# Kernel optimization log

Hardware: AMD Instinct MI355X
Metric: run time of the kernel (lower is better)

The kernel has to match this reference:

```python
import jax, jax.numpy as jnp
import numpy as np

B, T, C, H, N = 4, 1024, 1024, 16, 64
DW, DA, DV, DG = 64, 64, 64, 160  # LoRA ranks derived from C=1024
LNX_EPS = 0.00064


def layer_norm(h, g, b, eps=1e-5):
    m = h.mean(-1, keepdims=True)
    var = ((h - m) ** 2).mean(-1, keepdims=True)
    return (h - m) * jax.lax.rsqrt(var + eps) * g + b


def token_shift(h):
    # nn.ZeroPad2d((0,0,1,-1)): shift right along T, zero at t=0
    return jnp.pad(h, ((0, 0), (1, 0), (0, 0)))[:, :-1]


def wkv7(r, w, k, v, a, b):
    # RWKV-7 generalized recurrence. Inputs [B,T,C]; w is log-space decay.
    def re(t):
        return t.reshape(B, T, H, N).transpose(1, 0, 2, 3)  # -> [T,B,H,N]
    r, w, k, v, a, b = map(re, (r, w, k, v, a, b))
    dec = jnp.exp(-jnp.exp(w))
    S0 = jnp.zeros((B, H, N, N), r.dtype)  # state: [value_dim, key_dim]
    def step(S, ins):
        r_, d_, k_, v_, a_, b_ = ins
        sa = jnp.einsum('bhij,bhj->bhi', S, a_)
        S = S * d_[:, :, None, :] + sa[..., None] * b_[:, :, None, :] + v_[..., None] * k_[:, :, None, :]
        return S, jnp.einsum('bhij,bhj->bhi', S, r_)
    _, out = jax.lax.scan(step, S0, (r, dec, k, v, a, b))
    return out.transpose(1, 0, 2, 3).reshape(B, T, C)


def _forward(x, v_first, ln1_g, ln1_b, ln2_g, ln2_b, x_r, x_w, x_k_mix, x_v_mix, x_a, x_g,
             w0, w1, w2, a0, a1, a2, v0, v1, v2, g1, g2, k_k, k_a, r_k,
             W_r, W_k, W_v, W_o, lnx_g, lnx_b, xk_c, Wk_ff, Wv_ff):
    # ---- RNW_Tmix (original RWKV-7 path, layer_id > 0) ----
    h = layer_norm(x, ln1_g, ln1_b)
    xx = token_shift(h) - h
    xr = h + xx * x_r
    xw = h + xx * x_w
    xk = h + xx * x_k_mix
    xv = h + xx * x_v_mix
    xa = h + xx * x_a
    xg = h + xx * x_g
    r = xr @ W_r.T
    w = -jax.nn.softplus(-(w0 + jnp.tanh(xw @ w1) @ w2)) - 0.5
    k = xk @ W_k.T
    v = xv @ W_v.T
    v = v + (v_first - v) * jax.nn.sigmoid(v0 + (xv @ v1) @ v2)
    a = jax.nn.sigmoid(a0 + (xa @ a1) @ a2)
    g = jax.nn.sigmoid(xg @ g1) @ g2
    kk = (k * k_k).reshape(B, T, H, N)
    kk = kk / jnp.maximum(jnp.linalg.norm(kk, axis=-1, keepdims=True), 1e-12)
    kk = kk.reshape(B, T, C)
    k = k * (1 + (a - 1) * k_a)
    y = wkv7(r, w, k, v, -kk, kk * a)
    # GroupNorm(H groups of N channels), eps=0.00064
    yg = y.reshape(B, T, H, N)
    m = yg.mean(-1, keepdims=True)
    var = ((yg - m) ** 2).mean(-1, keepdims=True)
    y = ((yg - m) * jax.lax.rsqrt(var + LNX_EPS)).reshape(B, T, C) * lnx_g + lnx_b
    r4 = r.reshape(B, T, H, N)
    k4 = k.reshape(B, T, H, N)
    v4 = v.reshape(B, T, H, N)
    y = y + ((r4 * k4 * r_k).sum(-1, keepdims=True) * v4).reshape(B, T, C)
    x = x + (y * g) @ W_o.T
    # ---- RWKV_CMix_x070 ----
    h2 = layer_norm(x, ln2_g, ln2_b)
    hx = token_shift(h2) - h2
    kf = h2 + hx * xk_c
    kf = jnp.square(jax.nn.relu(kf @ Wk_ff.T))
    x = x + kf @ Wv_ff.T
    return x


def setup_inputs() -> dict:
    key = jax.random.key(0)
    ks = jax.random.split(key, 40)
    it = iter(range(40))
    def rn(shape, s=0.02):
        return (jax.random.normal(ks[next(it)], shape) * s).astype(jnp.float32)
    def ru(shape):
        return jax.random.uniform(ks[next(it)], shape).astype(jnp.float32)
    return {
        'x': rn((B, T, C), 1.0),
        'v_first': rn((B, T, C), 1.0),
        'ln1_g': jnp.ones((C,), jnp.float32), 'ln1_b': jnp.zeros((C,), jnp.float32),
        'ln2_g': jnp.ones((C,), jnp.float32), 'ln2_b': jnp.zeros((C,), jnp.float32),
        'x_r': ru((1, 1, C)), 'x_w': ru((1, 1, C)), 'x_k_mix': ru((1, 1, C)),
        'x_v_mix': ru((1, 1, C)), 'x_a': ru((1, 1, C)), 'x_g': ru((1, 1, C)),
        'w0': rn((1, 1, C), 0.5) - 4.0, 'w1': rn((C, DW)), 'w2': rn((DW, C), 0.1),
        'a0': rn((1, 1, C), 0.3), 'a1': rn((C, DA)), 'a2': rn((DA, C), 0.1),
        'v0': rn((1, 1, C), 0.3) + 0.73, 'v1': rn((C, DV)), 'v2': rn((DV, C), 0.1),
        'g1': rn((C, DG)), 'g2': rn((DG, C), 0.1),
        'k_k': rn((1, 1, C), 0.05) + 0.71, 'k_a': rn((1, 1, C), 0.05) + 1.02,
        'r_k': rn((H, N), 0.05) - 0.04,
        'W_r': rn((C, C)), 'W_k': rn((C, C), 0.002), 'W_v': rn((C, C)), 'W_o': rn((C, C)),
        'lnx_g': jnp.ones((C,), jnp.float32), 'lnx_b': jnp.zeros((C,), jnp.float32),
        'xk_c': ru((1, 1, C)),
        'Wk_ff': rn((4 * C, C)), 'Wv_ff': rn((C, 4 * C)),
    }


def reference(x, v_first, ln1_g, ln1_b, ln2_g, ln2_b, x_r, x_w, x_k_mix, x_v_mix, x_a, x_g,
              w0, w1, w2, a0, a1, a2, v0, v1, v2, g1, g2, k_k, k_a, r_k,
              W_r, W_k, W_v, W_o, lnx_g, lnx_b, xk_c, Wk_ff, Wv_ff):
    return _forward(x, v_first, ln1_g, ln1_b, ln2_g, ln2_b, x_r, x_w, x_k_mix, x_v_mix, x_a, x_g,
                    w0, w1, w2, a0, a1, a2, v0, v1, v2, g1, g2, k_k, k_a, r_k,
                    W_r, W_k, W_v, W_o, lnx_g, lnx_b, xk_c, Wk_ff, Wv_ff)
```

## Files before the change

kernel.cpp:

```cpp
#include <hip/hip_runtime.h>
#include <hip/hip_bf16.h>


#define BB 4
#define TT 1024
#define CC 1024
#define HH 16
#define NHEAD 64
#define MTOK 4096
#define FFDIM 4096

using bf16 = __hip_bfloat16;
typedef __attribute__((ext_vector_type(8))) short short8;
typedef __attribute__((ext_vector_type(4))) float f32x4;

__device__ __forceinline__ float b2f(bf16 x) { return __bfloat162float(x); }
__device__ __forceinline__ bf16 f2b(float x) { return __float2bfloat16(x); }
__device__ __forceinline__ float u2f(unsigned short u) {
  return __uint_as_float((unsigned)u << 16);
}
__device__ __forceinline__ float4 cv4(ushort4 u) {
  return make_float4(u2f(u.x), u2f(u.y), u2f(u.z), u2f(u.w));
}
__device__ __forceinline__ float ldin(const void* p, size_t i, int m) {
  return m ? b2f(((const bf16*)p)[i]) : ((const float*)p)[i];
}

__device__ __forceinline__ void async16(const void* g, void* l) {
  __builtin_amdgcn_global_load_lds((const __attribute__((address_space(1))) void*)g,
                                   (__attribute__((address_space(3))) void*)l, 16, 0, 0);
}

__device__ __forceinline__ float rowsum16(float x) {
  int t;
  t = __builtin_amdgcn_update_dpp(0, __float_as_int(x), 0x121, 0xF, 0xF, true);
  x += __int_as_float(t);
  t = __builtin_amdgcn_update_dpp(0, __float_as_int(x), 0x122, 0xF, 0xF, true);
  x += __int_as_float(t);
  t = __builtin_amdgcn_update_dpp(0, __float_as_int(x), 0x124, 0xF, 0xF, true);
  x += __int_as_float(t);
  t = __builtin_amdgcn_update_dpp(0, __float_as_int(x), 0x128, 0xF, 0xF, true);
  x += __int_as_float(t);
  return x;
}

__device__ __forceinline__ void rowsum16_2(float& x, float& y) {
  int t1, t2;
  t1 = __builtin_amdgcn_update_dpp(0, __float_as_int(x), 0x121, 0xF, 0xF, true);
  t2 = __builtin_amdgcn_update_dpp(0, __float_as_int(y), 0x121, 0xF, 0xF, true);
  x += __int_as_float(t1); y += __int_as_float(t2);
  t1 = __builtin_amdgcn_update_dpp(0, __float_as_int(x), 0x122, 0xF, 0xF, true);
  t2 = __builtin_amdgcn_update_dpp(0, __float_as_int(y), 0x122, 0xF, 0xF, true);
  x += __int_as_float(t1); y += __int_as_float(t2);
  t1 = __builtin_amdgcn_update_dpp(0, __float_as_int(x), 0x124, 0xF, 0xF, true);
  t2 = __builtin_amdgcn_update_dpp(0, __float_as_int(y), 0x124, 0xF, 0xF, true);
  x += __int_as_float(t1); y += __int_as_float(t2);
  t1 = __builtin_amdgcn_update_dpp(0, __float_as_int(x), 0x128, 0xF, 0xF, true);
  t2 = __builtin_amdgcn_update_dpp(0, __float_as_int(y), 0x128, 0xF, 0xF, true);
  x += __int_as_float(t1); y += __int_as_float(t2);
}

__global__ void probe_kernel(const unsigned int* g, int* flag) {
  if (threadIdx.x == 0 && blockIdx.x == 0) {
    flag[0] = (g[0] == 0x3F800000u) ? 0 : 1;
    flag[1] = 1;
  }
}

__global__ __launch_bounds__(256) void cvt_all(
    const void* wr, const void* wk, const void* wv, const void* wo,
    const void* wkff, const void* wvff, const int* flagp,
    bf16* wrc, bf16* wkc, bf16* wvc, bf16* woc, bf16* wkffc, bf16* wvffc) {
  const int z = blockIdx.z;
  const void* in; bf16* out; int n4;
  const int nCC4 = CC * CC / 4, nFF4 = FFDIM * CC / 4;
  switch (z) {
    case 0: in = wr;   out = wrc;   n4 = nCC4; break;
    case 1: in = wk;   out = wkc;   n4 = nCC4; break;
    case 2: in = wv;   out = wvc;   n4 = nCC4; break;
    case 3: in = wo;   out = woc;   n4 = nCC4; break;
    case 4: in = wkff; out = wkffc; n4 = nFF4; break;
    default: in = wvff; out = wvffc; n4 = nFF4; break;
  }
  const int fl = *flagp;
  const int i4 = blockIdx.x * 256 + threadIdx.x;
  if (i4 >= n4) return;
  const size_t i = (size_t)i4 * 4;
#pragma unroll
  for (int e = 0; e < 4; ++e) out[i + e] = f2b(ldin(in, i + e, fl));
}

__global__ __launch_bounds__(256) void fillmark_kernel(unsigned short* out, int n) {
  const int i = blockIdx.x * 256 + threadIdx.x;
  if (i < n) out[i] = 0x3F80;
}

template<int XM>
__global__ __launch_bounds__(256) void ln_kernel(const void* __restrict__ x,
    const void* __restrict__ g, const void* __restrict__ be, const int* flagp,
    bf16* __restrict__ out, float eps) {
  const int fl = *flagp;
  const int xm = (XM < 0) ? fl : XM;
  const int tid = threadIdx.x;
  const size_t base = (size_t)blockIdx.x * CC + tid * 4;
  float v[4];
#pragma unroll
  for (int e = 0; e < 4; ++e) v[e] = ldin(x, base + e, xm);
  float s  = v[0] + v[1] + v[2] + v[3];
  float ss = v[0]*v[0] + v[1]*v[1] + v[2]*v[2] + v[3]*v[3];
#pragma unroll
  for (int m = 1; m <= 32; m <<= 1) { s += __shfl_xor(s, m); ss += __shfl_xor(ss, m); }
  __shared__ float red[8];
  const int wave = tid >> 6, lane = tid & 63;
  if (lane == 0) { red[wave] = s; red[4 + wave] = ss; }
  __syncthreads();
  s  = red[0] + red[1] + red[2] + red[3];
  ss = red[4] + red[5] + red[6] + red[7];
  const float mean = s * (1.0f / CC);
  const float var  = ss * (1.0f / CC) - mean * mean;
  const float rstd = rsqrtf(var + eps);
#pragma unroll
  for (int e = 0; e < 4; ++e) {
    const int c = tid * 4 + e;
    out[base + e] = f2b((v[e] - mean) * rstd * ldin(g, c, fl) + ldin(be, c, fl));
  }
}

__global__ __launch_bounds__(256) void addln_kernel(const void* __restrict__ x,
    const bf16* __restrict__ ob, const void* __restrict__ g,
    const void* __restrict__ be, const int* flagp,
    float* __restrict__ x1, bf16* __restrict__ h2, float eps) {
  const int fl = *flagp;
  const int tid = threadIdx.x;
  const size_t base = (size_t)blockIdx.x * CC + tid * 4;
  float v[4];
#pragma unroll
  for (int e = 0; e < 4; ++e) {
    v[e] = ldin(x, base + e, fl) + b2f(ob[base + e]);
    x1[base + e] = v[e];
  }
  float s  = v[0] + v[1] + v[2] + v[3];
  float ss = v[0]*v[0] + v[1]*v[1] + v[2]*v[2] + v[3]*v[3];
#pragma unroll
  for (int m = 1; m <= 32; m <<= 1) { s += __shfl_xor(s, m); ss += __shfl_xor(ss, m); }
  __shared__ float red[8];
  const int wave = tid >> 6, lane = tid & 63;
  if (lane == 0) { red[wave] = s; red[4 + wave] = ss; }
  __syncthreads();
  s  = red[0] + red[1] + red[2] + red[3];
  ss = red[4] + red[5] + red[6] + red[7];
  const float mean = s * (1.0f / CC);
  const float var  = ss * (1.0f / CC) - mean * mean;
  const float rstd = rsqrtf(var + eps);
#pragma unroll
  for (int e = 0; e < 4; ++e) {
    const int c = tid * 4 + e;
    h2[base + e] = f2b((v[e] - mean) * rstd * ldin(g, c, fl) + ldin(be, c, fl));
  }
}

__global__ __launch_bounds__(256) void mix6_kernel(const bf16* __restrict__ h,
    const void* cr, const void* cw, const void* ck,
    const void* cv, const void* ca, const void* cg, const int* flagp,
    bf16* __restrict__ xr, bf16* __restrict__ xw, bf16* __restrict__ xk,
    bf16* __restrict__ xv, bf16* __restrict__ xa, bf16* __restrict__ xg) {
  const int fl = *flagp;
  const size_t idx = (size_t)blockIdx.x * 256 + threadIdx.x;
  const int c = idx & (CC - 1);
  const int t = (idx >> 10) & (TT - 1);
  const float hv = b2f(h[idx]);
  const float xx = (t == 0 ? 0.f : b2f(h[idx - CC])) - hv;
  xr[idx] = f2b(hv + xx * ldin(cr, c, fl));
  xw[idx] = f2b(hv + xx * ldin(cw, c, fl));
  xk[idx] = f2b(hv + xx * ldin(ck, c, fl));
  xv[idx] = f2b(hv + xx * ldin(cv, c, fl));
  xa[idx] = f2b(hv + xx * ldin(ca, c, fl));
  xg[idx] = f2b(hv + xx * ldin(cg, c, fl));
}

__global__ __launch_bounds__(256) void mix1_kernel(const bf16* __restrict__ h,
    const void* cf, const int* flagp, bf16* __restrict__ out) {
  const int fl = *flagp;
  const size_t idx = (size_t)blockIdx.x * 256 + threadIdx.x;
  const int c = idx & (CC - 1);
  const int t = (idx >> 10) & (TT - 1);
  const float hv = b2f(h[idx]);
  const float xx = (t == 0 ? 0.f : b2f(h[idx - CC])) - hv;
  out[idx] = f2b(hv + xx * ldin(cf, c, fl));
}

__global__ __launch_bounds__(256) void transpose_all(
    const void* w1, const void* a1, const void* v1, const void* g1,
    const void* w2, const void* a2, const void* v2, const void* g2,
    const int* flagp,
    bf16* w1t, bf16* a1t, bf16* v1t, bf16* g1t,
    bf16* w2t, bf16* a2t, bf16* v2t, bf16* g2t) {
  const int z = blockIdx.z;
  const void* in; bf16* out; int R, Cc;
  switch (z) {
    case 0: in = w1; out = w1t; R = CC;  Cc = 64;  break;
    case 1: in = a1; out = a1t; R = CC;  Cc = 64;  break;
    case 2: in = v1; out = v1t; R = CC;  Cc = 64;  break;
    case 3: in = g1; out = g1t; R = CC;  Cc = 160; break;
    case 4: in = w2; out = w2t; R = 64;  Cc = CC;  break;
    case 5: in = a2; out = a2t; R = 64;  Cc = CC;  break;
    case 6: in = v2; out = v2t; R = 64;  Cc = CC;  break;
    default: in = g2; out = g2t; R = 160; Cc = CC; break;
  }
  const int fl = *flagp;
  const int idx = blockIdx.x * 256 + threadIdx.x;
  if (idx >= R * Cc) return;
  const int r = idx / Cc, c = idx - r * Cc;
  out[(size_t)c * R + r] = f2b(ldin(in, idx, fl));
}

__device__ __forceinline__ void gemm_core(const bf16* __restrict__ A,
    const bf16* __restrict__ Bm, bf16* __restrict__ Out, int M, int N, int K,
    int lda, int ldb, int mode, short* As, short* Bs) {
  const int tid  = threadIdx.x;
  const int wave = tid >> 6;
  const int lane = tid & 63;
  const int m0 = blockIdx.y * 128;
  const int n0 = blockIdx.x * 128;
  const int wr = (wave >> 1) * 64;
  const int wc = (wave & 1) * 64;
  const int lrow = lane & 15;
  const int lq   = lane >> 4;
  f32x4 acc[4][4];
#pragma unroll
  for (int i = 0; i < 4; ++i)
#pragma unroll
    for (int j = 0; j < 4; ++j) acc[i][j] = (f32x4){0.f, 0.f, 0.f, 0.f};

  for (int k0 = 0; k0 < K; k0 += 32) {
#pragma unroll
    for (int j = 0; j < 2; ++j) {
      const int chunk = j * 256 + tid;
      const int row = chunk >> 2;
      const int c8  = (chunk & 3) * 8;
      const int ldsbase = (j * 256 + wave * 64) * 8;
      const bf16* ga = A + (size_t)(m0 + row) * lda + (k0 + c8);
      int br = n0 + row; br = br < N ? br : N - 1;
      const bf16* gb = Bm + (size_t)br * ldb + (k0 + c8);
      async16(ga, &As[ldsbase]);
      async16(gb, &Bs[ldsbase]);
    }
    __syncthreads();
    short8 af[4], bfr[4];
#pragma unroll
    for (int mi = 0; mi < 4; ++mi)
      af[mi] = *(const short8*)&As[(wr + mi * 16 + lrow) * 32 + lq * 8];
#pragma unroll
    for (int ni = 0; ni < 4; ++ni)
      bfr[ni] = *(const short8*)&Bs[(wc + ni * 16 + lrow) * 32 + lq * 8];
#pragma unroll
    for (int mi = 0; mi < 4; ++mi)
#pragma unroll
      for (int ni = 0; ni < 4; ++ni)
        acc[mi][ni] = __builtin_amdgcn_mfma_f32_16x16x32_bf16(af[mi], bfr[ni], acc[mi][ni], 0, 0, 0);
    __syncthreads();
  }
#pragma unroll
  for (int mi = 0; mi < 4; ++mi) {
#pragma unroll
    for (int ni = 0; ni < 4; ++ni) {
      const int col = n0 + wc + ni * 16 + lrow;
      if (col < N) {
#pragma unroll
        for (int rr = 0; rr < 4; ++rr) {
          const int rowg = m0 + wr + mi * 16 + lq * 4 + rr;
          const size_t oidx = (size_t)rowg * N + col;
          const float val = acc[mi][ni][rr];
          if (mode == 1) { const float t = val > 0.f ? val : 0.f; Out[oidx] = f2b(t * t); }
          else if (mode == 2) Out[oidx] = f2b(val);
          else if (mode == 3) Out[oidx] = f2b(tanhf(val));
          else if (mode == 4) Out[oidx] = f2b(1.f / (1.f + expf(-val)));
          else ((float*)Out)[oidx] = val;
        }
      }
    }
  }
}

template<int MODE>
__global__ __launch_bounds__(256) void gemm_mf(const bf16* __restrict__ A,
    const bf16* __restrict__ Bm, bf16* __restrict__ Out, int M, int N, int K) {
  __shared__ short As[128 * 32];
  __shared__ short Bs[128 * 32];
  gemm_core(A, Bm, Out, M, N, K, K, K, MODE, As, Bs);
}

__global__ __launch_bounds__(256) void gemm_qkl(
    const bf16* xw, const bf16* xa, const bf16* xv, const bf16* xg,
    const bf16* xr, const bf16* xk,
    const bf16* w1t, const bf16* a1t, const bf16* v1t, const bf16* g1t,
    const bf16* wrc, const bf16* wkc,
    bf16* wm, bf16* am, bf16* vm, bf16* gm,
    bf16* rb, bf16* kg) {
  __shared__ short As[128 * 32];
  __shared__ short Bs[128 * 32];
  const int z = blockIdx.z;
  const bf16* A; const bf16* B; bf16* O; int N; int mode;
  if (z == 0)      { A = xw;  B = w1t; O = wm; N = 64;  mode = 3; }
  else if (z == 1) { A = xa;  B = a1t; O = am; N = 64;  mode = 2; }
  else if (z == 2) { A = xv;  B = v1t; O = vm; N = 64;  mode = 2; }
  else if (z == 3) { A = xg;  B = g1t; O = gm; N = 160; mode = 4; }
  else if (z == 4) { A = xr;  B = wrc; O = rb; N = CC;  mode = 2; }
  else             { A = xk;  B = wkc; O = kg; N = CC;  mode = 2; }
  if ((int)blockIdx.x * 128 >= N) return;
  gemm_core(A, B, O, MTOK, N, CC, CC, CC, mode, As, Bs);
}

__global__ __launch_bounds__(256) void gemm_lora2v(
    const bf16* wm, const bf16* am, const bf16* vm, const bf16* gm,
    const bf16* xv,
    const bf16* w2t, const bf16* a2t, const bf16* v2t, const bf16* g2t,
    const bf16* wvc,
    bf16* wl, bf16* al, bf16* vl, bf16* gb, bf16* vg) {
  __shared__ short As[128 * 32];
  __shared__ short Bs[128 * 32];
  const int z = blockIdx.z;
  const bf16* A; const bf16* B; bf16* O; int K;
  if (z == 0)      { A = wm; B = w2t; O = wl; K = 64;  }
  else if (z == 1) { A = am; B = a2t; O = al; K = 64;  }
  else if (z == 2) { A = vm; B = v2t; O = vl; K = 64;  }
  else if (z == 3) { A = gm; B = g2t; O = gb; K = 160; }
  else             { A = xv; B = wvc; O = vg; K = CC;  }
  gemm_core(A, B, O, MTOK, CC, K, K, K, 2, As, Bs);
}

__global__ __launch_bounds__(256) void gemm_ff2sk(
    const bf16* __restrict__ kact, const bf16* __restrict__ wvffc,
    float* p0, float* p1) {
  __shared__ short As[128 * 32];
  __shared__ short Bs[128 * 32];
  const int z = blockIdx.z;
  const int koff = z * (FFDIM / 2);
  float* P = z ? p1 : p0;
  gemm_core(kact + koff, wvffc + koff, (bf16*)P, MTOK, CC, FFDIM / 2,
            FFDIM, FFDIM, 5, As, Bs);
}

template<int MODE>
__global__ __launch_bounds__(256) void gemm_bt(const bf16* __restrict__ A,
    const void* __restrict__ Bm, const int* bmp, bf16* __restrict__ Out,
    int M, int N, int K) {
  const int bm = *bmp;
  __shared__ float As[64][17];
  __shared__ float Bs[64][17];
  const int tid = threadIdx.x;
  const int m0 = blockIdx.y * 64;
  const int n0 = blockIdx.x * 64;
  const int ty = tid >> 4, tx = tid & 15;
  float acc[4][4] = {};
  for (int k0 = 0; k0 < K; k0 += 16) {
    __syncthreads();
#pragma unroll
    for (int e = 0; e < 4; ++e) {
      const int lin = e * 256 + tid;
      const int row = lin >> 4;
      const int kk  = lin & 15;
      As[row][kk] = b2f(A[(size_t)(m0 + row) * K + k0 + kk]);
      int br = n0 + row; br = br < N ? br : N - 1;
      Bs[row][kk] = ldin(Bm, (size_t)br * K + k0 + kk, bm);
    }
    __syncthreads();
#pragma unroll
    for (int k = 0; k < 16; ++k) {
      float a[4], b[4];
#pragma unroll
      for (int i = 0; i < 4; ++i) a[i] = As[ty * 4 + i][k];
#pragma unroll
      for (int j = 0; j < 4; ++j) b[j] = Bs[tx * 4 + j][k];
#pragma unroll
      for (int i = 0; i < 4; ++i)
#pragma unroll
        for (int j = 0; j < 4; ++j) acc[i][j] += a[i] * b[j];
    }
  }
#pragma unroll
  for (int i = 0; i < 4; ++i) {
    const int rowg = m0 + ty * 4 + i;
#pragma unroll
    for (int j = 0; j < 4; ++j) {
      const int col = n0 + tx * 4 + j;
      if (col < N) {
        const size_t oidx = (size_t)rowg * N + col;
        const float val = acc[i][j];
        if (MODE == 1) { const float t = val > 0.f ? val : 0.f; Out[oidx] = f2b(t * t); }
        else if (MODE == 2) Out[oidx] = f2b(val);
        else if (MODE == 3) Out[oidx] = f2b(tanhf(val));
        else Out[oidx] = f2b(1.f / (1.f + expf(-val)));
      }
    }
  }
}

__global__ __launch_bounds__(256) void combine_kernel(
    bf16* kf, bf16* vf, bf16* wl, bf16* al, bf16* vl,
    const void* vfirst, const void* w0, const void* a0, const void* v0,
    const void* kkp, const void* kap, const int* flagp, float* decp) {
  const int fl = *flagp;
  const int tid = threadIdx.x;
  const size_t base = (size_t)blockIdx.x * CC + tid * 4;
  float kkv[4], av4[4];
  float ssq = 0.f;
#pragma unroll
  for (int e = 0; e < 4; ++e) {
    const int c = tid * 4 + e;
    const size_t idx = base + e;
    const float u = ldin(w0, c, fl) + b2f(wl[idx]);
    const float w = (u > 0.f ? -log1pf(expf(-u)) : u - log1pf(expf(u))) - 0.5f;
    wl[idx] = f2b(w);
    if (decp) decp[idx] = __expf(-__expf(w));
    const float a  = 1.f / (1.f + expf(-(ldin(a0, c, fl) + b2f(al[idx]))));
    const float vg = 1.f / (1.f + expf(-(ldin(v0, c, fl) + b2f(vl[idx]))));
    const float v = b2f(vf[idx]);
    vf[idx] = f2b(v + (ldin(vfirst, idx, fl) - v) * vg);
    const float kv = b2f(kf[idx]);
    const float kkr = kv * ldin(kkp, c, fl);
    kkv[e] = kkr; av4[e] = a;
    ssq += kkr * kkr;
    kf[idx] = f2b(kv * (1.f + (a - 1.f) * ldin(kap, c, fl)));
  }
  ssq += __shfl_xor(ssq, 1); ssq += __shfl_xor(ssq, 2);
  ssq += __shfl_xor(ssq, 4); ssq += __shfl_xor(ssq, 8);
  const float inv = 1.f / fmaxf(sqrtf(ssq), 1e-12f);
#pragma unroll
  for (int e = 0; e < 4; ++e) {
    const size_t idx = base + e;
    const float kkn = kkv[e] * inv;
    al[idx] = f2b(-kkn);
    vl[idx] = f2b(kkn * av4[e]);
  }
}


template<int DF>
__device__ __forceinline__ void wkv_stage(const bf16* rp, const void* wp,
    const bf16* kp, const bf16* vp, const bf16* ap, const bf16* bp,
    size_t cb, char* sb, int wave, int lane) {
  const int hb = wave & 1;
  const size_t g2 = cb + (size_t)(hb * 8 + (lane >> 3)) * CC + (lane & 7) * 8;
  if (wave < 2) {
    async16(rp + g2, sb + 0    + hb * 1024);
    async16(kp + g2, sb + 2048 + hb * 1024);
    async16(ap + g2, sb + 4096 + hb * 1024);
  } else {
    async16(bp + g2, sb + 6144 + hb * 1024);
    async16(vp + g2, sb + 8192 + hb * 1024);
  }
  if constexpr (DF) {
    const size_t gd = cb + (size_t)(wave * 4 + (lane >> 4)) * CC + (lane & 15) * 4;
    async16((const float*)wp + gd, sb + 10240 + wave * 1024);
  } else {
    if (wave >= 2) async16((const bf16*)wp + g2, sb + 10240 + hb * 1024);
  }
}

template<int DF>
__device__ __forceinline__ void wkv_load_step(const char* sb, int t, int j0, int i,
    float4& rv, float4& dv, float4& av, float4& bv, float4& vk) {
  const short* sR = (const short*)sb;
  const short* sK = (const short*)(sb + 2048);
  const short* sA = (const short*)(sb + 4096);
  const short* sB = (const short*)(sb + 6144);
  const unsigned short* sV = (const unsigned short*)(sb + 8192);
  rv = cv4(*(const ushort4*)(const void*)(sR + t * 64 + j0));
  const float4 kv = cv4(*(const ushort4*)(const void*)(sK + t * 64 + j0));
  av = cv4(*(const ushort4*)(const void*)(sA + t * 64 + j0));
  bv = cv4(*(const ushort4*)(const void*)(sB + t * 64 + j0));
  const float vi = u2f(sV[t * 64 + i]);
  if constexpr (DF) {
    const float* sD = (const float*)(sb + 10240);
    dv = *(const float4*)(const void*)(sD + t * 64 + j0);
  } else {
    const short* sW = (const short*)(sb + 10240);
    const float4 wv = cv4(*(const ushort4*)(const void*)(sW + t * 64 + j0));
    dv = make_float4(__expf(-__expf(wv.x)), __expf(-__expf(wv.y)),
                     __expf(-__expf(wv.z)), __expf(-__expf(wv.w)));
  }
  vk = make_float4(vi * kv.x, vi * kv.y, vi * kv.z, vi * kv.w);
}

template<int DF>
__global__ __launch_bounds__(256) void wkv_scan(
    const bf16* __restrict__ rp, const void* __restrict__ wp,
    const bf16* __restrict__ kp, const bf16* __restrict__ vp,
    const bf16* __restrict__ ap, const bf16* __restrict__ bp,
    bf16* __restrict__ yp) {
  constexpr int BUFB = DF ? 14336 : 12288;
  __shared__ char sbuf[2][BUFB];
  const int blk = blockIdx.x;
  const int q = blk & 3;
  const int h = (blk >> 2) & (HH - 1);
  const int b = blk >> 6;
  const int tid = threadIdx.x;
  const int wave = tid >> 6;
  const int lane = tid & 63;
  const int rl = tid >> 4;
  const int jq = tid & 15;
  const int j0 = jq * 4;
  const int i = q * 16 + rl;
  const size_t bbase = (size_t)b * TT * CC + (size_t)h * NHEAD;

  float4 S = make_float4(0.f, 0.f, 0.f, 0.f);

  wkv_stage<DF>(rp, wp, kp, vp, ap, bp, bbase, sbuf[0], wave, lane);
  __syncthreads();

  for (int c = 0; c < TT / 16; ++c) {
    if (c + 1 < TT / 16)
      wkv_stage<DF>(rp, wp, kp, vp, ap, bp, bbase + (size_t)(c + 1) * 16 * CC,
                    sbuf[(c + 1) & 1], wave, lane);
    const char* sb = sbuf[c & 1];

    float4 rv, dv, av, bv, vk;
    wkv_load_step<DF>(sb, 0, j0, i, rv, dv, av, bv, vk);
    float qv_prev = 0.f;
    float ocol = 0.f;
#pragma unroll
    for (int s = 0; s < 16; ++s) {
      float4 rv2, dv2, av2, bv2, vk2;
      if (s + 1 < 16)
        wkv_load_step<DF>(sb, s + 1, j0, i, rv2, dv2, av2, bv2, vk2);
      float p = (S.x * av.x + S.y * av.y) + (S.z * av.z + S.w * av.w);
      if (s == 0) {
        p = rowsum16(p);
      } else {
        rowsum16_2(p, qv_prev);
        ocol = (jq == s - 1) ? qv_prev : ocol;
      }
      const float sa = p;
      S.x = fmaf(S.x, dv.x, fmaf(sa, bv.x, vk.x));
      S.y = fmaf(S.y, dv.y, fmaf(sa, bv.y, vk.y));
      S.z = fmaf(S.z, dv.z, fmaf(sa, bv.z, vk.z));
      S.w = fmaf(S.w, dv.w, fmaf(sa, bv.w, vk.w));
      qv_prev = (S.x * rv.x + S.y * rv.y) + (S.z * rv.z + S.w * rv.w);
      if (s + 1 < 16) { rv = rv2; dv = dv2; av = av2; bv = bv2; vk = vk2; }
    }
    qv_prev = rowsum16(qv_prev);
    ocol = (jq == 15) ? qv_prev : ocol;
    yp[bbase + (size_t)(c * 16 + jq) * CC + i] = f2b(ocol);
    __syncthreads();
  }
}

__global__ __launch_bounds__(256) void post_kernel(
    const bf16* __restrict__ y, const bf16* __restrict__ rp, const bf16* __restrict__ kp,
    const bf16* __restrict__ vp, const bf16* __restrict__ gp,
    const void* rk, const void* lnxg, const void* lnxb, const int* flagp,
    bf16* __restrict__ out) {
  const int fl = *flagp;
  const int tid = threadIdx.x;
  const size_t base = (size_t)blockIdx.x * CC + tid * 4;
  float yv[4];
  float s = 0.f, ssq = 0.f, dot = 0.f;
#pragma unroll
  for (int e = 0; e < 4; ++e) {
    const size_t idx = base + e;
    yv[e] = b2f(y[idx]);
    s += yv[e]; ssq += yv[e] * yv[e];
    dot += b2f(rp[idx]) * b2f(kp[idx]) * ldin(rk, tid * 4 + e, fl);
  }
  s   += __shfl_xor(s, 1);   s   += __shfl_xor(s, 2);   s   += __shfl_xor(s, 4);   s   += __shfl_xor(s, 8);
  ssq += __shfl_xor(ssq, 1); ssq += __shfl_xor(ssq, 2); ssq += __shfl_xor(ssq, 4); ssq += __shfl_xor(ssq, 8);
  dot += __shfl_xor(dot, 1); dot += __shfl_xor(dot, 2); dot += __shfl_xor(dot, 4); dot += __shfl_xor(dot, 8);
  const float m = s * (1.f / NHEAD);
  const float var = ssq * (1.f / NHEAD) - m * m;
  const float rs = rsqrtf(var + 0.00064f);
#pragma unroll
  for (int e = 0; e < 4; ++e) {
    const int c = tid * 4 + e;
    const size_t idx = base + e;
    const float yo = (yv[e] - m) * rs * ldin(lnxg, c, fl) + ldin(lnxb, c, fl)
                     + dot * b2f(vp[idx]);
    out[idx] = f2b(yo * b2f(gp[idx]));
  }
}

__global__ __launch_bounds__(256) void addres_kernel(const void* x, const int* flagp,
    const bf16* __restrict__ o, float* __restrict__ out) {
  const int fl = *flagp;
  const size_t idx = (size_t)blockIdx.x * 256 + threadIdx.x;
  out[idx] = ldin(x, idx, fl) + b2f(o[idx]);
}

__global__ __launch_bounds__(256) void final_kernel(const float* __restrict__ x1,
    const bf16* __restrict__ f, const int* flagp, void* out) {
  const int fl = *flagp;
  const size_t idx = (size_t)blockIdx.x * 256 + threadIdx.x;
  const float v = x1[idx] + b2f(f[idx]);
  if (fl) ((bf16*)out)[idx] = f2b(v);
  else    ((float*)out)[idx] = v;
}

__global__ __launch_bounds__(256) void final_sk_kernel(const float* __restrict__ x1,
    const float* __restrict__ p0, const float* __restrict__ p1,
    const int* flagp, void* out) {
  const int fl = *flagp;
  const size_t idx = (size_t)blockIdx.x * 256 + threadIdx.x;
  const float v = x1[idx] + (p0[idx] + p1[idx]);
  if (fl) ((bf16*)out)[idx] = f2b(v);
  else    ((float*)out)[idx] = v;
}

extern "C" void kernel_launch(void* const* d_in, const int* in_sizes, int n_in,
                              void* d_out, int out_size, void* d_ws, size_t ws_size,
                              hipStream_t stream) {
  const void* X      = d_in[0];
  const void* VFIRST = d_in[1];
  const void* LN1G = d_in[2];
  const void* LN1B = d_in[3];
  const void* LN2G = d_in[4];
  const void* LN2B = d_in[5];
  const void* XRC = d_in[6];
  const void* XWC = d_in[7];
  const void* XKC = d_in[8];
  const void* XVC = d_in[9];
  const void* XAC = d_in[10];
  const void* XGC = d_in[11];
  const void* W0p = d_in[12];
  const void* W1p = d_in[13];
  const void* W2p = d_in[14];
  const void* A0p = d_in[15];
  const void* A1p = d_in[16];
  const void* A2p = d_in[17];
  const void* V0p = d_in[18];
  const void* V1p = d_in[19];
  const void* V2p = d_in[20];
  const void* G1p = d_in[21];
  const void* G2p = d_in[22];
  const void* KKp = d_in[23];
  const void* KAp = d_in[24];
  const void* RKp = d_in[25];
  const void* WR  = d_in[26];
  const void* WK  = d_in[27];
  const void* WV  = d_in[28];
  const void* WO  = d_in[29];
  const void* LNXG = d_in[30];
  const void* LNXB = d_in[31];
  const void* XKCF = d_in[32];
  const void* WKFF = d_in[33];
  const void* WVFF = d_in[34];

  const size_t BTC  = (size_t)MTOK * CC;
  const size_t SLOT = BTC * 2;
  char* ws = (char*)d_ws;

  size_t off = 8 * SLOT;
  auto alloc = [&](size_t n) { size_t o = off; off += (n + 255) & ~(size_t)255; return o; };
  const size_t oW1T = alloc((size_t)CC * 64 * 2);
  const size_t oA1T = alloc((size_t)CC * 64 * 2);
  const size_t oV1T = alloc((size_t)CC * 64 * 2);
  const size_t oG1T = alloc((size_t)CC * 160 * 2);
  const size_t oW2T = alloc((size_t)CC * 64 * 2);
  const size_t oA2T = alloc((size_t)CC * 64 * 2);
  const size_t oV2T = alloc((size_t)CC * 64 * 2);
  const size_t oG2T = alloc((size_t)CC * 160 * 2);
  const size_t oWM  = alloc((size_t)MTOK * 64 * 2);
  const size_t oAM  = alloc((size_t)MTOK * 64 * 2);
  const size_t oVM  = alloc((size_t)MTOK * 64 * 2);
  const size_t oGM  = alloc((size_t)MTOK * 160 * 2);
  const size_t oFLG = alloc(8);
  const size_t baseNeed = off;
  const size_t oDEC = alloc(BTC * 4);
  const size_t decNeed = off;
  const size_t oWRc   = alloc((size_t)CC * CC * 2);
  const size_t oWKc   = alloc((size_t)CC * CC * 2);
  const size_t oWVc   = alloc((size_t)CC * CC * 2);
  const size_t oWOc   = alloc((size_t)CC * CC * 2);
  const size_t oWKFFc = alloc((size_t)FFDIM * CC * 2);
  const size_t oWVFFc = alloc((size_t)CC * FFDIM * 2);
  const size_t mfmaNeed = off;
  const size_t oP0 = alloc(BTC * 4);
  const size_t oP1 = alloc(BTC * 4);
  const size_t ff2Need = off;

  if (baseNeed > ws_size) {
    fillmark_kernel<<<(out_size + 255) / 256, 256, 0, stream>>>(
        (unsigned short*)d_out, out_size);
    return;
  }
  const bool hasdec = (decNeed <= ws_size);
  const bool useMF  = (mfmaNeed <= ws_size);
  const bool hasff2 = (ff2Need <= ws_size);

  int* FLAG = (int*)(ws + oFLG);
  int* ONE  = FLAG + 1;

  bf16* B0 = (bf16*)(ws + 0 * SLOT);
  bf16* B1 = (bf16*)(ws + 1 * SLOT);
  bf16* B2 = (bf16*)(ws + 2 * SLOT);
  bf16* B3 = (bf16*)(ws + 3 * SLOT);
  bf16* B4 = (bf16*)(ws + 4 * SLOT);
  bf16* B5 = (bf16*)(ws + 5 * SLOT);
  bf16* B6 = (bf16*)(ws + 6 * SLOT);
  bf16* B7 = (bf16*)(ws + 7 * SLOT);
  bf16* Hb  = B0;
  bf16* XRb = B1; bf16* XWb = B2; bf16* XKb = B3;
  bf16* XVb = B4; bf16* XAb = B5; bf16* XGb = B6;
  bf16* Rb  = B7;
  bf16* Kg  = B0;
  bf16* Vg  = B1;
  bf16* WLb = B2;
  bf16* ALb = B3;
  bf16* VLb = B6;
  bf16* Gb  = B5;
  bf16* Yb  = B4;
  bf16* YG  = B2;
  bf16* OBb = B0;
  float* X1b = (float*)(ws + 2 * SLOT);
  bf16* H2b  = B1;
  bf16* KFIN = B0;
  bf16* KACT = B4;
  bf16* FFNb = B1;

  bf16* W1T = (bf16*)(ws + oW1T);
  bf16* A1T = (bf16*)(ws + oA1T);
  bf16* V1T = (bf16*)(ws + oV1T);
  bf16* G1T = (bf16*)(ws + oG1T);
  bf16* W2T = (bf16*)(ws + oW2T);
  bf16* A2T = (bf16*)(ws + oA2T);
  bf16* V2T = (bf16*)(ws + oV2T);
  bf16* G2T = (bf16*)(ws + oG2T);
  bf16* WM  = (bf16*)(ws + oWM);
  bf16* AM  = (bf16*)(ws + oAM);
  bf16* VM  = (bf16*)(ws + oVM);
  bf16* GM  = (bf16*)(ws + oGM);
  float* DECb = (float*)(ws + oDEC);
  float* DECarg = hasdec ? DECb : (float*)nullptr;
  bf16* WRc   = (bf16*)(ws + oWRc);
  bf16* WKc   = (bf16*)(ws + oWKc);
  bf16* WVc   = (bf16*)(ws + oWVc);
  bf16* WOc   = (bf16*)(ws + oWOc);
  bf16* WKFFc = (bf16*)(ws + oWKFFc);
  bf16* WVFFc = (bf16*)(ws + oWVFFc);
  float* P0 = (float*)(ws + oP0);
  float* P1 = (float*)(ws + oP1);

  const int EW = (int)(BTC / 256);
  const dim3 blk256(256);

  probe_kernel<<<1, 1, 0, stream>>>((const unsigned int*)LN1G, FLAG);

  ln_kernel<-1><<<MTOK, blk256, 0, stream>>>(X, LN1G, LN1B, FLAG, Hb, 1e-5f);
  mix6_kernel<<<EW, blk256, 0, stream>>>(Hb, XRC, XWC, XKC, XVC, XAC, XGC, FLAG,
                                         XRb, XWb, XKb, XVb, XAb, XGb);
  transpose_all<<<dim3(640, 1, 8), blk256, 0, stream>>>(
      W1p, A1p, V1p, G1p, W2p, A2p, V2p, G2p, FLAG,
      W1T, A1T, V1T, G1T, W2T, A2T, V2T, G2T);

  if (useMF) {
    cvt_all<<<dim3(4096, 1, 6), blk256, 0, stream>>>(
        WR, WK, WV, WO, WKFF, WVFF, FLAG, WRc, WKc, WVc, WOc, WKFFc, WVFFc);

    const dim3 gCC(8, 32), gFF1(32, 32);
    gemm_qkl<<<dim3(8, 32, 6), blk256, 0, stream>>>(
        XWb, XAb, XVb, XGb, XRb, XKb,
        W1T, A1T, V1T, G1T, WRc, WKc,
        WM, AM, VM, GM, Rb, Kg);
    gemm_lora2v<<<dim3(8, 32, 5), blk256, 0, stream>>>(
        WM, AM, VM, GM, XVb,
        W2T, A2T, V2T, G2T, WVc,
        WLb, ALb, VLb, Gb, Vg);

    combine_kernel<<<MTOK, blk256, 0, stream>>>(Kg, Vg, WLb, ALb, VLb, VFIRST,
                                                W0p, A0p, V0p, KKp, KAp, FLAG, DECarg);
    if (hasdec)
      wkv_scan<1><<<BB * HH * 4, blk256, 0, stream>>>(Rb, DECb, Kg, Vg, ALb, VLb, Yb);
    else
      wkv_scan<0><<<BB * HH * 4, blk256, 0, stream>>>(Rb, WLb, Kg, Vg, ALb, VLb, Yb);
    post_kernel<<<MTOK, blk256, 0, stream>>>(Yb, Rb, Kg, Vg, Gb, RKp, LNXG, LNXB, FLAG, YG);
    gemm_mf<2><<<gCC, blk256, 0, stream>>>(YG, WOc, OBb, MTOK, CC, CC);
    addln_kernel<<<MTOK, blk256, 0, stream>>>(X, OBb, LN2G, LN2B, FLAG, X1b, H2b, 1e-5f);

    mix1_kernel<<<EW, blk256, 0, stream>>>(H2b, XKCF, FLAG, KFIN);
    gemm_mf<1><<<gFF1, blk256, 0, stream>>>(KFIN, WKFFc, KACT, MTOK, FFDIM, CC);
    if (hasff2) {
      gemm_ff2sk<<<dim3(8, 32, 2), blk256, 0, stream>>>(KACT, WVFFc, P0, P1);
      final_sk_kernel<<<EW, blk256, 0, stream>>>(X1b, P0, P1, FLAG, d_out);
    } else {
      gemm_mf<2><<<gCC, blk256, 0, stream>>>(KACT, WVFFc, FFNb, MTOK, CC, FFDIM);
      final_kernel<<<EW, blk256, 0, stream>>>(X1b, FFNb, FLAG, d_out);
    }
  } else {
    const dim3 gCC(16, 64), gL1(1, 64), gG1(3, 64), gFF1(64, 64);
    gemm_bt<3><<<gL1, blk256, 0, stream>>>(XWb, W1T, ONE, WM, MTOK, 64, CC);
    gemm_bt<2><<<gL1, blk256, 0, stream>>>(XAb, A1T, ONE, AM, MTOK, 64, CC);
    gemm_bt<2><<<gL1, blk256, 0, stream>>>(XVb, V1T, ONE, VM, MTOK, 64, CC);
    gemm_bt<4><<<gG1, blk256, 0, stream>>>(XGb, G1T, ONE, GM, MTOK, 160, CC);
    gemm_bt<2><<<gCC, blk256, 0, stream>>>(XRb, WR, FLAG, Rb, MTOK, CC, CC);
    gemm_bt<2><<<gCC, blk256, 0, stream>>>(XKb, WK, FLAG, Kg, MTOK, CC, CC);
    gemm_bt<2><<<gCC, blk256, 0, stream>>>(XVb, WV, FLAG, Vg, MTOK, CC, CC);
    gemm_bt<2><<<gCC, blk256, 0, stream>>>(WM, W2T, ONE, WLb, MTOK, CC, 64);
    gemm_bt<2><<<gCC, blk256, 0, stream>>>(AM, A2T, ONE, ALb, MTOK, CC, 64);
    gemm_bt<2><<<gCC, blk256, 0, stream>>>(VM, V2T, ONE, VLb, MTOK, CC, 64);
    gemm_bt<2><<<gCC, blk256, 0, stream>>>(GM, G2T, ONE, Gb, MTOK, CC, 160);

    combine_kernel<<<MTOK, blk256, 0, stream>>>(Kg, Vg, WLb, ALb, VLb, VFIRST,
                                                W0p, A0p, V0p, KKp, KAp, FLAG, DECarg);
    if (hasdec)
      wkv_scan<1><<<BB * HH * 4, blk256, 0, stream>>>(Rb, DECb, Kg, Vg, ALb, VLb, Yb);
    else
      wkv_scan<0><<<BB * HH * 4, blk256, 0, stream>>>(Rb, WLb, Kg, Vg, ALb, VLb, Yb);
    post_kernel<<<MTOK, blk256, 0, stream>>>(Yb, Rb, Kg, Vg, Gb, RKp, LNXG, LNXB, FLAG, YG);
    gemm_bt<2><<<gCC, blk256, 0, stream>>>(YG, WO, FLAG, OBb, MTOK, CC, CC);
    addln_kernel<<<MTOK, blk256, 0, stream>>>(X, OBb, LN2G, LN2B, FLAG, X1b, H2b, 1e-5f);

    mix1_kernel<<<EW, blk256, 0, stream>>>(H2b, XKCF, FLAG, KFIN);
    gemm_bt<1><<<gFF1, blk256, 0, stream>>>(KFIN, WKFF, FLAG, KACT, MTOK, FFDIM, CC);
    gemm_bt<2><<<gCC, blk256, 0, stream>>>(KACT, WVFF, FLAG, FFNb, MTOK, CC, FFDIM);
    final_kernel<<<EW, blk256, 0, stream>>>(X1b, FFNb, FLAG, d_out);
  }

  (void)in_sizes; (void)n_in; (void)out_size;
}
```

Measured before the change: 774.6 us.

## Overlap WKV scan with g-LoRA GEMM and late weight conversions in one launch

A single fused kernel dispatches on block index. The first 256 blocks run the latency-bound WKV recurrence, the next 256 run the g2 LoRA GEMM, and the remaining blocks convert the W_o and FFN weights to bf16. Those two jobs are removed from the earlier cvt_all and gemm_lora2v launches, so they can fill CUs left idle by the sequential scan instead of sitting on the critical path. The fused kernel always uses the decay-buffer (DF=1) scan variant, so the non-precomputed decay branch is dropped. Shared-memory sizing now follows the larger scan buffer for every block.

After: 762.4 us. Within noise of the previous version (-1.6%).

```diff
diff --git a/kernel.cpp b/kernel.cpp
--- a/kernel.cpp
+++ b/kernel.cpp
@@ -68,24 +68,15 @@
 }
 
 __global__ __launch_bounds__(256) void cvt_all(
-    const void* wr, const void* wk, const void* wv, const void* wo,
-    const void* wkff, const void* wvff, const int* flagp,
-    bf16* wrc, bf16* wkc, bf16* wvc, bf16* woc, bf16* wkffc, bf16* wvffc) {
+    const void* wr, const void* wk, const void* wv, const int* flagp,
+    bf16* wrc, bf16* wkc, bf16* wvc) {
   const int z = blockIdx.z;
-  const void* in; bf16* out; int n4;
-  const int nCC4 = CC * CC / 4, nFF4 = FFDIM * CC / 4;
-  switch (z) {
-    case 0: in = wr;   out = wrc;   n4 = nCC4; break;
-    case 1: in = wk;   out = wkc;   n4 = nCC4; break;
-    case 2: in = wv;   out = wvc;   n4 = nCC4; break;
-    case 3: in = wo;   out = woc;   n4 = nCC4; break;
-    case 4: in = wkff; out = wkffc; n4 = nFF4; break;
-    default: in = wvff; out = wvffc; n4 = nFF4; break;
-  }
-  const int fl = *flagp;
-  const int i4 = blockIdx.x * 256 + threadIdx.x;
-  if (i4 >= n4) return;
-  const size_t i = (size_t)i4 * 4;
+  const void* in; bf16* out;
+  if (z == 0)      { in = wr; out = wrc; }
+  else if (z == 1) { in = wk; out = wkc; }
+  else             { in = wv; out = wvc; }
+  const int fl = *flagp;
+  const size_t i = ((size_t)blockIdx.x * 256 + threadIdx.x) * 4;
 #pragma unroll
   for (int e = 0; e < 4; ++e) out[i + e] = f2b(ldin(in, i + e, fl));
 }
@@ -216,12 +207,12 @@
 
 __device__ __forceinline__ void gemm_core(const bf16* __restrict__ A,
     const bf16* __restrict__ Bm, bf16* __restrict__ Out, int M, int N, int K,
-    int lda, int ldb, int mode, short* As, short* Bs) {
+    int lda, int ldb, int mode, short* As, short* Bs, int bm, int bn) {
   const int tid  = threadIdx.x;
   const int wave = tid >> 6;
   const int lane = tid & 63;
-  const int m0 = blockIdx.y * 128;
-  const int n0 = blockIdx.x * 128;
+  const int m0 = bm * 128;
+  const int n0 = bn * 128;
   const int wr = (wave >> 1) * 64;
   const int wc = (wave & 1) * 64;
   const int lrow = lane & 15;
@@ -287,7 +278,7 @@
     const bf16* __restrict__ Bm, bf16* __restrict__ Out, int M, int N, int K) {
   __shared__ short As[128 * 32];
   __shared__ short Bs[128 * 32];
-  gemm_core(A, Bm, Out, M, N, K, K, K, MODE, As, Bs);
+  gemm_core(A, Bm, Out, M, N, K, K, K, MODE, As, Bs, blockIdx.y, blockIdx.x);
 }
 
 __global__ __launch_bounds__(256) void gemm_qkl(
@@ -308,15 +299,15 @@
   else if (z == 4) { A = xr;  B = wrc; O = rb; N = CC;  mode = 2; }
   else             { A = xk;  B = wkc; O = kg; N = CC;  mode = 2; }
   if ((int)blockIdx.x * 128 >= N) return;
-  gemm_core(A, B, O, MTOK, N, CC, CC, CC, mode, As, Bs);
+  gemm_core(A, B, O, MTOK, N, CC, CC, CC, mode, As, Bs, blockIdx.y, blockIdx.x);
 }
 
 __global__ __launch_bounds__(256) void gemm_lora2v(
-    const bf16* wm, const bf16* am, const bf16* vm, const bf16* gm,
+    const bf16* wm, const bf16* am, const bf16* vm,
     const bf16* xv,
-    const bf16* w2t, const bf16* a2t, const bf16* v2t, const bf16* g2t,
+    const bf16* w2t, const bf16* a2t, const bf16* v2t,
     const bf16* wvc,
-    bf16* wl, bf16* al, bf16* vl, bf16* gb, bf16* vg) {
+    bf16* wl, bf16* al, bf16* vl, bf16* vg) {
   __shared__ short As[128 * 32];
   __shared__ short Bs[128 * 32];
   const int z = blockIdx.z;
@@ -324,9 +315,8 @@
   if (z == 0)      { A = wm; B = w2t; O = wl; K = 64;  }
   else if (z == 1) { A = am; B = a2t; O = al; K = 64;  }
   else if (z == 2) { A = vm; B = v2t; O = vl; K = 64;  }
-  else if (z == 3) { A = gm; B = g2t; O = gb; K = 160; }
   else             { A = xv; B = wvc; O = vg; K = CC;  }
-  gemm_core(A, B, O, MTOK, CC, K, K, K, 2, As, Bs);
+  gemm_core(A, B, O, MTOK, CC, K, K, K, 2, As, Bs, blockIdx.y, blockIdx.x);
 }
 
 __global__ __launch_bounds__(256) void gemm_ff2sk(
@@ -338,7 +328,7 @@
   const int koff = z * (FFDIM / 2);
   float* P = z ? p1 : p0;
   gemm_core(kact + koff, wvffc + koff, (bf16*)P, MTOK, CC, FFDIM / 2,
-            FFDIM, FFDIM, 5, As, Bs);
+            FFDIM, FFDIM, 5, As, Bs, blockIdx.y, blockIdx.x);
 }
 
 template<int MODE>
@@ -484,14 +474,12 @@
 }
 
 template<int DF>
-__global__ __launch_bounds__(256) void wkv_scan(
+__device__ __forceinline__ void wkv_scan_body(char* sbase, int blk,
     const bf16* __restrict__ rp, const void* __restrict__ wp,
     const bf16* __restrict__ kp, const bf16* __restrict__ vp,
     const bf16* __restrict__ ap, const bf16* __restrict__ bp,
     bf16* __restrict__ yp) {
   constexpr int BUFB = DF ? 14336 : 12288;
-  __shared__ char sbuf[2][BUFB];
-  const int blk = blockIdx.x;
   const int q = blk & 3;
   const int h = (blk >> 2) & (HH - 1);
   const int b = blk >> 6;
@@ -506,14 +494,14 @@
 
   float4 S = make_float4(0.f, 0.f, 0.f, 0.f);
 
-  wkv_stage<DF>(rp, wp, kp, vp, ap, bp, bbase, sbuf[0], wave, lane);
+  wkv_stage<DF>(rp, wp, kp, vp, ap, bp, bbase, sbase, wave, lane);
   __syncthreads();
 
   for (int c = 0; c < TT / 16; ++c) {
     if (c + 1 < TT / 16)
       wkv_stage<DF>(rp, wp, kp, vp, ap, bp, bbase + (size_t)(c + 1) * 16 * CC,
-                    sbuf[(c + 1) & 1], wave, lane);
-    const char* sb = sbuf[c & 1];
+                    sbase + ((c + 1) & 1) * BUFB, wave, lane);
+    const char* sb = sbase + (c & 1) * BUFB;
 
     float4 rv, dv, av, bv, vk;
     wkv_load_step<DF>(sb, 0, j0, i, rv, dv, av, bv, vk);
@@ -543,6 +531,47 @@
     ocol = (jq == 15) ? qv_prev : ocol;
     yp[bbase + (size_t)(c * 16 + jq) * CC + i] = f2b(ocol);
     __syncthreads();
+  }
+}
+
+template<int DF>
+__global__ __launch_bounds__(256) void wkv_scan(
+    const bf16* __restrict__ rp, const void* __restrict__ wp,
+    const bf16* __restrict__ kp, const bf16* __restrict__ vp,
+    const bf16* __restrict__ ap, const bf16* __restrict__ bp,
+    bf16* __restrict__ yp) {
+  __shared__ char sbuf[2 * (DF ? 14336 : 12288)];
+  wkv_scan_body<DF>(sbuf, blockIdx.x, rp, wp, kp, vp, ap, bp, yp);
+}
+
+#define FUSED_GRID (256 + 256 + 1024 + 4096 + 4096)
+__global__ __launch_bounds__(256) void scan_fused(
+    const bf16* __restrict__ rp, const float* __restrict__ decp,
+    const bf16* __restrict__ kp, const bf16* __restrict__ vp,
+    const bf16* __restrict__ ap, const bf16* __restrict__ bp,
+    bf16* __restrict__ yp,
+    const bf16* __restrict__ gm, const bf16* __restrict__ g2t,
+    bf16* __restrict__ gbuf,
+    const void* wo, const void* wkff, const void* wvff, const int* flagp,
+    bf16* woc, bf16* wkffc, bf16* wvffc) {
+  __shared__ char smem[2 * 14336];
+  const int bx = blockIdx.x;
+  if (bx < 256) {
+    wkv_scan_body<1>(smem, bx, rp, decp, kp, vp, ap, bp, yp);
+  } else if (bx < 512) {
+    const int gb = bx - 256;
+    gemm_core(gm, g2t, gbuf, MTOK, CC, 160, 160, 160, 2,
+              (short*)smem, (short*)(smem + 8192), gb >> 3, gb & 7);
+  } else {
+    const int fl = *flagp;
+    int bc = bx - 512;
+    const void* in; bf16* out;
+    if (bc < 1024)      { in = wo;   out = woc; }
+    else if (bc < 5120) { in = wkff; out = wkffc; bc -= 1024; }
+    else                { in = wvff; out = wvffc; bc -= 5120; }
+    const size_t i = ((size_t)bc * 256 + threadIdx.x) * 4;
+#pragma unroll
+    for (int e = 0; e < 4; ++e) out[i + e] = f2b(ldin(in, i + e, fl));
   }
 }
 
@@ -752,25 +781,25 @@
       W1T, A1T, V1T, G1T, W2T, A2T, V2T, G2T);
 
   if (useMF) {
-    cvt_all<<<dim3(4096, 1, 6), blk256, 0, stream>>>(
-        WR, WK, WV, WO, WKFF, WVFF, FLAG, WRc, WKc, WVc, WOc, WKFFc, WVFFc);
+    cvt_all<<<dim3(1024, 1, 3), blk256, 0, stream>>>(
+        WR, WK, WV, FLAG, WRc, WKc, WVc);
 
     const dim3 gCC(8, 32), gFF1(32, 32);
     gemm_qkl<<<dim3(8, 32, 6), blk256, 0, stream>>>(
         XWb, XAb, XVb, XGb, XRb, XKb,
         W1T, A1T, V1T, G1T, WRc, WKc,
         WM, AM, VM, GM, Rb, Kg);
-    gemm_lora2v<<<dim3(8, 32, 5), blk256, 0, stream>>>(
-        WM, AM, VM, GM, XVb,
-        W2T, A2T, V2T, G2T, WVc,
-        WLb, ALb, VLb, Gb, Vg);
+    gemm_lora2v<<<dim3(8, 32, 4), blk256, 0, stream>>>(
+        WM, AM, VM, XVb,
+        W2T, A2T, V2T, WVc,
+        WLb, ALb, VLb, Vg);
 
     combine_kernel<<<MTOK, blk256, 0, stream>>>(Kg, Vg, WLb, ALb, VLb, VFIRST,
                                                 W0p, A0p, V0p, KKp, KAp, FLAG, DECarg);
-    if (hasdec)
-      wkv_scan<1><<<BB * HH * 4, blk256, 0, stream>>>(Rb, DECb, Kg, Vg, ALb, VLb, Yb);
-    else
-      wkv_scan<0><<<BB * HH * 4, blk256, 0, stream>>>(Rb, WLb, Kg, Vg, ALb, VLb, Yb);
+    scan_fused<<<FUSED_GRID, blk256, 0, stream>>>(
+        Rb, DECb, Kg, Vg, ALb, VLb, Yb,
+        GM, G2T, Gb,
+        WO, WKFF, WVFF, FLAG, WOc, WKFFc, WVFFc);
     post_kernel<<<MTOK, blk256, 0, stream>>>(Yb, Rb, Kg, Vg, Gb, RKp, LNXG, LNXB, FLAG, YG);
     gemm_mf<2><<<gCC, blk256, 0, stream>>>(YG, WOc, OBb, MTOK, CC, CC);
     addln_kernel<<<MTOK, blk256, 0, stream>>>(X, OBb, LN2G, LN2B, FLAG, X1b, H2b, 1e-5f);
```
